# Kernel tuning notes

Hardware: AMD Instinct MI355X
Metric: run time of the kernel (lower is better)

Reference implementation:

```python
import jax, jax.numpy as jnp
import numpy as np

ALPHA = 32.0
RANK = 16.0

def setup_inputs() -> dict:
    key = jax.random.key(0)
    k1, k2, k3, k4, k5 = jax.random.split(key, 5)
    B_, S, D_in, D_out, r = 4, 2048, 4096, 4096, 16
    x = jax.random.normal(k1, (B_, S, D_in), dtype=jnp.float32)
    W = jax.random.normal(k2, (D_out, D_in), dtype=jnp.float32) * 0.02
    b = jax.random.normal(k3, (D_out,), dtype=jnp.float32) * 0.02
    lora_A = jax.random.normal(k4, (r, D_in), dtype=jnp.float32) * 0.01
    lora_B = jax.random.normal(k5, (D_out, r), dtype=jnp.float32) * 0.01
    return {"x": x, "W": W, "b": b, "lora_A": lora_A, "lora_B": lora_B}

def reference(x, W, b, lora_A, lora_B):
    # frozen linear: x @ W^T + b
    base = jnp.einsum('bsd,od->bso', x, W) + b
    # LoRA delta computed sequentially (same math as F.linear(x, B@A)):
    # (alpha/rank) * (x @ A^T) @ B^T  -- avoids materializing [out,in]
    xa = jnp.einsum('bsd,rd->bsr', x, lora_A)      # [B,S,r]
    lora = jnp.einsum('bsr,or->bso', xa, lora_B)   # [B,S,out]
    scale = ALPHA / RANK
    # dropout p=0.0 (eval / deterministic) -> identity
    return base + scale * lora
```

## Files before the change

kernel.cpp:

```cpp
#include <hip/hip_runtime.h>


static constexpr int Mdim = 8192;
static constexpr int Ndim = 4096;
static constexpr int Kdim = 4096;
#define LORA_SCALE 2.0f

typedef __bf16 bf16;
typedef __bf16 bf16x8 __attribute__((ext_vector_type(8)));
typedef __bf16 bf16x4 __attribute__((ext_vector_type(4)));
typedef float f32x4 __attribute__((ext_vector_type(4)));

__device__ __forceinline__ void gload_lds16(const void* g, void* l) {
  __builtin_amdgcn_global_load_lds(
      (const __attribute__((address_space(1))) unsigned int*)g,
      (__attribute__((address_space(3))) unsigned int*)l, 16, 0, 0);
}

__global__ __launch_bounds__(256) void cvt_x_kernel(const float* __restrict__ x,
                                                    bf16* __restrict__ xb, int n8) {
  for (int i = blockIdx.x * blockDim.x + threadIdx.x; i < n8;
       i += gridDim.x * blockDim.x) {
    const float4* p = reinterpret_cast<const float4*>(x) + (size_t)i * 2;
    float4 a = p[0];
    float4 c = p[1];
    bf16x8 o;
    o[0] = (bf16)a.x; o[1] = (bf16)a.y; o[2] = (bf16)a.z; o[3] = (bf16)a.w;
    o[4] = (bf16)c.x; o[5] = (bf16)c.y; o[6] = (bf16)c.z; o[7] = (bf16)c.w;
    reinterpret_cast<bf16x8*>(xb)[i] = o;
  }
}

__global__ __launch_bounds__(256) void build_w_kernel(const float* __restrict__ W,
                                                      const float* __restrict__ lA,
                                                      const float* __restrict__ lB,
                                                      bf16* __restrict__ wb) {
  const int n0 = blockIdx.x * 8;
  const int t = threadIdx.x;
  __shared__ float bs[8][16];
  if (t < 128) bs[t >> 4][t & 15] = lB[(n0 + (t >> 4)) * 16 + (t & 15)] * LORA_SCALE;
  __syncthreads();
  for (int k0 = t * 4; k0 < Kdim; k0 += 1024) {
    float4 acc[8];
#pragma unroll
    for (int j = 0; j < 8; ++j)
      acc[j] = *reinterpret_cast<const float4*>(&W[(size_t)(n0 + j) * Kdim + k0]);
#pragma unroll
    for (int r = 0; r < 16; ++r) {
      float4 a = *reinterpret_cast<const float4*>(&lA[r * Kdim + k0]);
#pragma unroll
      for (int j = 0; j < 8; ++j) {
        acc[j].x += bs[j][r] * a.x;
        acc[j].y += bs[j][r] * a.y;
        acc[j].z += bs[j][r] * a.z;
        acc[j].w += bs[j][r] * a.w;
      }
    }
#pragma unroll
    for (int j = 0; j < 8; ++j) {
      bf16x4 o;
      o[0] = (bf16)acc[j].x; o[1] = (bf16)acc[j].y;
      o[2] = (bf16)acc[j].z; o[3] = (bf16)acc[j].w;
      *reinterpret_cast<bf16x4*>(&wb[(size_t)(n0 + j) * Kdim + k0]) = o;
    }
  }
}

__global__ __launch_bounds__(512, 2) void gemm8(const bf16* __restrict__ Xb,
                                                const bf16* __restrict__ Wb,
                                                const float* __restrict__ bias,
                                                float* __restrict__ out) {
  extern __shared__ char smem[];
  const int tid = threadIdx.x;
  const int lane = tid & 63;
  const int wid = tid >> 6;
  const int wm = wid >> 2, wn = wid & 3;
  const int r16 = lane & 15;
  const int kq = lane >> 4;

  const int wg = blockIdx.x;
  const int swz = (wg & 7) * 64 + (wg >> 3);
  const int bm0 = (swz & 31) * 256;
  const int bn0 = (swz >> 5) * 256;

  const int aBase = wm * 16384 + kq * 2048 + r16 * 16;
  const int bBase = 32768 + (wn >> 1) * 16384 + kq * 2048 + ((wn & 1) * 64 + r16) * 16;

  const bf16* aRow = Xb + (size_t)(bm0 + (tid & 127)) * Kdim + (tid >> 7) * 8;
  const bf16* bRow = Wb + (size_t)(bn0 + (tid & 127)) * Kdim + (tid >> 7) * 8;

  auto stageA = [&](int kt, int h, char* buf) {
    const bf16* s = aRow + (size_t)h * 128 * Kdim + kt * 64;
    char* d = buf + h * 16384 + tid * 16;
    gload_lds16(s, d);
    gload_lds16(s + 32, d + 8192);
  };
  auto stageB = [&](int kt, int h, char* buf) {
    const bf16* s = bRow + (size_t)h * 128 * Kdim + kt * 64;
    char* d = buf + 32768 + h * 16384 + tid * 16;
    gload_lds16(s, d);
    gload_lds16(s + 32, d + 8192);
  };
#define ABUF(d) (smem + (d) * 65536)

  f32x4 acc[8][4] = {};
  bf16x8 a0[8], a1[8], b0[4], b1[4];

  stageA(0, 0, ABUF(0));
  stageA(0, 1, ABUF(0));
  stageB(0, 0, ABUF(0));
  stageB(0, 1, ABUF(0));
  stageA(1, 0, ABUF(1));
  stageA(1, 1, ABUF(1));

  for (int t = 0; t < 64; ++t) {
    if (t == 63) {
      asm volatile("s_waitcnt vmcnt(0)" ::: "memory");
    } else {
      asm volatile("s_waitcnt vmcnt(4)" ::: "memory");
    }
    __builtin_amdgcn_s_barrier();
    char* Ab = ABUF(t & 1);

#pragma unroll
    for (int mi = 0; mi < 8; ++mi)
      a0[mi] = *reinterpret_cast<const bf16x8*>(Ab + aBase + mi * 256);
#pragma unroll
    for (int nj = 0; nj < 4; ++nj)
      b0[nj] = *reinterpret_cast<const bf16x8*>(Ab + bBase + nj * 256);
    if (t < 63) stageB(t + 1, 0, ABUF((t + 1) & 1));
    __builtin_amdgcn_s_barrier();
    asm volatile("s_waitcnt lgkmcnt(0)" ::: "memory");
    __builtin_amdgcn_sched_barrier(0);
    __builtin_amdgcn_s_setprio(1);
#pragma unroll
    for (int mi = 0; mi < 4; ++mi)
#pragma unroll
      for (int nj = 0; nj < 4; ++nj)
        acc[mi][nj] = __builtin_amdgcn_mfma_f32_16x16x32_bf16(a0[mi], b0[nj],
                                                              acc[mi][nj], 0, 0, 0);
    __builtin_amdgcn_s_setprio(0);
    __builtin_amdgcn_s_barrier();

#pragma unroll
    for (int mi = 0; mi < 8; ++mi)
      a1[mi] = *reinterpret_cast<const bf16x8*>(Ab + 8192 + aBase + mi * 256);
#pragma unroll
    for (int nj = 0; nj < 4; ++nj)
      b1[nj] = *reinterpret_cast<const bf16x8*>(Ab + 8192 + bBase + nj * 256);
    if (t < 63) stageB(t + 1, 1, ABUF((t + 1) & 1));
    __builtin_amdgcn_s_barrier();
    asm volatile("s_waitcnt lgkmcnt(0)" ::: "memory");
    __builtin_amdgcn_sched_barrier(0);
    __builtin_amdgcn_s_setprio(1);
#pragma unroll
    for (int mi = 4; mi < 8; ++mi)
#pragma unroll
      for (int nj = 0; nj < 4; ++nj)
        acc[mi][nj] = __builtin_amdgcn_mfma_f32_16x16x32_bf16(a0[mi], b0[nj],
                                                              acc[mi][nj], 0, 0, 0);
    __builtin_amdgcn_s_setprio(0);
    __builtin_amdgcn_s_barrier();

    if (t < 62) stageA(t + 2, 0, Ab);
    __builtin_amdgcn_s_setprio(1);
#pragma unroll
    for (int mi = 0; mi < 4; ++mi)
#pragma unroll
      for (int nj = 0; nj < 4; ++nj)
        acc[mi][nj] = __builtin_amdgcn_mfma_f32_16x16x32_bf16(a1[mi], b1[nj],
                                                              acc[mi][nj], 0, 0, 0);
    __builtin_amdgcn_s_setprio(0);

    if (t < 62) stageA(t + 2, 1, Ab);
    __builtin_amdgcn_s_setprio(1);
#pragma unroll
    for (int mi = 4; mi < 8; ++mi)
#pragma unroll
      for (int nj = 0; nj < 4; ++nj)
        acc[mi][nj] = __builtin_amdgcn_mfma_f32_16x16x32_bf16(a1[mi], b1[nj],
                                                              acc[mi][nj], 0, 0, 0);
    __builtin_amdgcn_s_setprio(0);
  }

  const int crow0 = bm0 + wm * 128 + (lane >> 4) * 4;
  const int ccol0 = bn0 + wn * 64 + r16;
#pragma unroll
  for (int nj = 0; nj < 4; ++nj) {
    float bv = bias[ccol0 + nj * 16];
#pragma unroll
    for (int mi = 0; mi < 8; ++mi)
#pragma unroll
      for (int r = 0; r < 4; ++r)
        out[(size_t)(crow0 + mi * 16 + r) * Ndim + ccol0 + nj * 16] =
            acc[mi][nj][r] + bv;
  }
#undef ABUF
}

__global__ __launch_bounds__(256) void gemm_fallback(const float* __restrict__ x,
                                                     const float* __restrict__ W,
                                                     const float* __restrict__ bias,
                                                     const float* __restrict__ lA,
                                                     const float* __restrict__ lB,
                                                     float* __restrict__ out) {
  __shared__ float xs[16][64];
  __shared__ float wt[16][64];
  const int t = threadIdx.x;
  const int tx = t & 15, ty = t >> 4;
  const int bm0 = blockIdx.y * 64, bn0 = blockIdx.x * 64;
  float acc[4][4] = {};
  for (int kt = 0; kt < Kdim; kt += 16) {
    __syncthreads();
    for (int e = t; e < 1024; e += 256) {
      int m = e >> 4, k = e & 15;
      xs[k][m] = x[(size_t)(bm0 + m) * Kdim + kt + k];
    }
    for (int e = t; e < 1024; e += 256) {
      int n = e >> 4, k = e & 15;
      float v = W[(size_t)(bn0 + n) * Kdim + kt + k];
#pragma unroll
      for (int r = 0; r < 16; ++r)
        v += LORA_SCALE * lB[(bn0 + n) * 16 + r] * lA[r * Kdim + kt + k];
      wt[k][n] = v;
    }
    __syncthreads();
#pragma unroll
    for (int k = 0; k < 16; ++k) {
      float xa[4], wv[4];
#pragma unroll
      for (int i = 0; i < 4; ++i) xa[i] = xs[k][ty * 4 + i];
#pragma unroll
      for (int j = 0; j < 4; ++j) wv[j] = wt[k][tx * 4 + j];
#pragma unroll
      for (int i = 0; i < 4; ++i)
#pragma unroll
        for (int j = 0; j < 4; ++j) acc[i][j] += xa[i] * wv[j];
    }
  }
#pragma unroll
  for (int i = 0; i < 4; ++i)
#pragma unroll
    for (int j = 0; j < 4; ++j)
      out[(size_t)(bm0 + ty * 4 + i) * Ndim + bn0 + tx * 4 + j] =
          acc[i][j] + bias[bn0 + tx * 4 + j];
}

extern "C" void kernel_launch(void* const* d_in, const int* in_sizes, int n_in,
                              void* d_out, int out_size, void* d_ws, size_t ws_size,
                              hipStream_t stream) {
  const float* x = (const float*)d_in[0];
  const float* W = (const float*)d_in[1];
  const float* b = (const float*)d_in[2];
  const float* lA = (const float*)d_in[3];
  const float* lB = (const float*)d_in[4];
  float* out = (float*)d_out;

  const size_t xb_bytes = (size_t)Mdim * Kdim * sizeof(bf16);
  const size_t wb_bytes = (size_t)Ndim * Kdim * sizeof(bf16);

  if (ws_size >= xb_bytes + wb_bytes) {
    bf16* xb = (bf16*)d_ws;
    bf16* wb = (bf16*)((char*)d_ws + xb_bytes);
    cvt_x_kernel<<<4096, 256, 0, stream>>>(x, xb, Mdim * Kdim / 8);
    build_w_kernel<<<Ndim / 8, 256, 0, stream>>>(W, lA, lB, wb);
    (void)hipFuncSetAttribute((const void*)gemm8,
                              hipFuncAttributeMaxDynamicSharedMemorySize, 131072);
    gemm8<<<dim3((Mdim / 256) * (Ndim / 256)), dim3(512), 131072, stream>>>(xb, wb, b,
                                                                            out);
  } else {
    dim3 grid(Ndim / 64, Mdim / 64);
    gemm_fallback<<<grid, 64 * 4, 0, stream>>>(x, W, b, lA, lB, out);
  }
}
```

Baseline: 378.7 us.

## Restructure gemm8 main loop to interleave A fragment reads with MFMA and drop barriers

```diff
diff --git a/kernel.cpp b/kernel.cpp
--- a/kernel.cpp
+++ b/kernel.cpp
@@ -65,6 +65,10 @@
     }
   }
 }
+
+#define LGKM0_FENCE                                              \
+  asm volatile("s_waitcnt lgkmcnt(0)" ::: "memory");             \
+  __builtin_amdgcn_sched_barrier(0);
 
 __global__ __launch_bounds__(512, 2) void gemm8(const bf16* __restrict__ Xb,
                                                 const bf16* __restrict__ Wb,
@@ -110,8 +114,8 @@
   stageA(0, 1, ABUF(0));
   stageB(0, 0, ABUF(0));
   stageB(0, 1, ABUF(0));
-  stageA(1, 0, ABUF(1));
-  stageA(1, 1, ABUF(1));
+  stageB(1, 0, ABUF(1));
+  stageB(1, 1, ABUF(1));
 
   for (int t = 0; t < 64; ++t) {
     if (t == 63) {
@@ -123,15 +127,13 @@
     char* Ab = ABUF(t & 1);
 
 #pragma unroll
-    for (int mi = 0; mi < 8; ++mi)
-      a0[mi] = *reinterpret_cast<const bf16x8*>(Ab + aBase + mi * 256);
-#pragma unroll
     for (int nj = 0; nj < 4; ++nj)
       b0[nj] = *reinterpret_cast<const bf16x8*>(Ab + bBase + nj * 256);
-    if (t < 63) stageB(t + 1, 0, ABUF((t + 1) & 1));
-    __builtin_amdgcn_s_barrier();
-    asm volatile("s_waitcnt lgkmcnt(0)" ::: "memory");
-    __builtin_amdgcn_sched_barrier(0);
+#pragma unroll
+    for (int mi = 0; mi < 4; ++mi)
+      a0[mi] = *reinterpret_cast<const bf16x8*>(Ab + aBase + mi * 256);
+    if (t < 63) stageA(t + 1, 0, ABUF((t + 1) & 1));
+    LGKM0_FENCE
     __builtin_amdgcn_s_setprio(1);
 #pragma unroll
     for (int mi = 0; mi < 4; ++mi)
@@ -140,47 +142,54 @@
         acc[mi][nj] = __builtin_amdgcn_mfma_f32_16x16x32_bf16(a0[mi], b0[nj],
                                                               acc[mi][nj], 0, 0, 0);
     __builtin_amdgcn_s_setprio(0);
-    __builtin_amdgcn_s_barrier();
-
-#pragma unroll
-    for (int mi = 0; mi < 8; ++mi)
-      a1[mi] = *reinterpret_cast<const bf16x8*>(Ab + 8192 + aBase + mi * 256);
+
 #pragma unroll
     for (int nj = 0; nj < 4; ++nj)
       b1[nj] = *reinterpret_cast<const bf16x8*>(Ab + 8192 + bBase + nj * 256);
-    if (t < 63) stageB(t + 1, 1, ABUF((t + 1) & 1));
+#pragma unroll
+    for (int mi = 4; mi < 8; ++mi)
+      a0[mi] = *reinterpret_cast<const bf16x8*>(Ab + aBase + mi * 256);
+    if (t < 63) stageA(t + 1, 1, ABUF((t + 1) & 1));
+    LGKM0_FENCE
+    __builtin_amdgcn_s_setprio(1);
+#pragma unroll
+    for (int mi = 4; mi < 8; ++mi)
+#pragma unroll
+      for (int nj = 0; nj < 4; ++nj)
+        acc[mi][nj] = __builtin_amdgcn_mfma_f32_16x16x32_bf16(a0[mi], b0[nj],
+                                                              acc[mi][nj], 0, 0, 0);
+    __builtin_amdgcn_s_setprio(0);
+    __builtin_amdgcn_sched_barrier(0);
     __builtin_amdgcn_s_barrier();
-    asm volatile("s_waitcnt lgkmcnt(0)" ::: "memory");
+
+#pragma unroll
+    for (int mi = 0; mi < 4; ++mi)
+      a1[mi] = *reinterpret_cast<const bf16x8*>(Ab + 8192 + aBase + mi * 256);
+    if (t < 62) stageB(t + 2, 0, Ab);
+    LGKM0_FENCE
+    __builtin_amdgcn_s_setprio(1);
+#pragma unroll
+    for (int mi = 0; mi < 4; ++mi)
+#pragma unroll
+      for (int nj = 0; nj < 4; ++nj)
+        acc[mi][nj] = __builtin_amdgcn_mfma_f32_16x16x32_bf16(a1[mi], b1[nj],
+                                                              acc[mi][nj], 0, 0, 0);
+    __builtin_amdgcn_s_setprio(0);
+
+#pragma unroll
+    for (int mi = 4; mi < 8; ++mi)
+      a1[mi] = *reinterpret_cast<const bf16x8*>(Ab + 8192 + aBase + mi * 256);
+    if (t < 62) stageB(t + 2, 1, Ab);
+    LGKM0_FENCE
+    __builtin_amdgcn_s_setprio(1);
+#pragma unroll
+    for (int mi = 4; mi < 8; ++mi)
+#pragma unroll
+      for (int nj = 0; nj < 4; ++nj)
+        acc[mi][nj] = __builtin_amdgcn_mfma_f32_16x16x32_bf16(a1[mi], b1[nj],
+                                                              acc[mi][nj], 0, 0, 0);
+    __builtin_amdgcn_s_setprio(0);
     __builtin_amdgcn_sched_barrier(0);
-    __builtin_amdgcn_s_setprio(1);
-#pragma unroll
-    for (int mi = 4; mi < 8; ++mi)
-#pragma unroll
-      for (int nj = 0; nj < 4; ++nj)
-        acc[mi][nj] = __builtin_amdgcn_mfma_f32_16x16x32_bf16(a0[mi], b0[nj],
-                                                              acc[mi][nj], 0, 0, 0);
-    __builtin_amdgcn_s_setprio(0);
-    __builtin_amdgcn_s_barrier();
-
-    if (t < 62) stageA(t + 2, 0, Ab);
-    __builtin_amdgcn_s_setprio(1);
-#pragma unroll
-    for (int mi = 0; mi < 4; ++mi)
-#pragma unroll
-      for (int nj = 0; nj < 4; ++nj)
-        acc[mi][nj] = __builtin_amdgcn_mfma_f32_16x16x32_bf16(a1[mi], b1[nj],
-                                                              acc[mi][nj], 0, 0, 0);
-    __builtin_amdgcn_s_setprio(0);
-
-    if (t < 62) stageA(t + 2, 1, Ab);
-    __builtin_amdgcn_s_setprio(1);
-#pragma unroll
-    for (int mi = 4; mi < 8; ++mi)
-#pragma unroll
-      for (int nj = 0; nj < 4; ++nj)
-        acc[mi][nj] = __builtin_amdgcn_mfma_f32_16x16x32_bf16(a1[mi], b1[nj],
-                                                              acc[mi][nj], 0, 0, 0);
-    __builtin_amdgcn_s_setprio(0);
   }
 
   const int crow0 = bm0 + wm * 128 + (lane >> 4) * 4;
```

New measurement: 381.1 us. Within noise of the previous version (+0.6%).
